# Kernel optimization log

Hardware: AMD Instinct MI355X
Metric: run time of the kernel (lower is better)

## Reference

```python
import jax, jax.numpy as jnp
import numpy as np

B, T, C, A, D, H, W = 2, 16, 64, 64, 32, 32, 32  # batch, timepoints, channels, att_features, spatial


def setup_inputs() -> dict:
    key = jax.random.key(0)
    ks = jax.random.split(key, 7)
    s = 1.0 / np.sqrt(C)
    return {
        "x": jax.random.normal(ks[0], (B, T, C, D, H, W), dtype=jnp.float32),
        "Wk": jax.random.normal(ks[1], (A, C), dtype=jnp.float32) * s,
        "bk": jax.random.normal(ks[2], (A,), dtype=jnp.float32) * s,
        "Wq": jax.random.normal(ks[3], (A, C), dtype=jnp.float32) * s,
        "bq": jax.random.normal(ks[4], (A,), dtype=jnp.float32) * s,
        "Wv": jax.random.normal(ks[5], (C, C), dtype=jnp.float32) * s,
        "bv": jax.random.normal(ks[6], (C,), dtype=jnp.float32) * s,
    }


def reference(x, Wk, bk, Wq, bq, Wv, bv):
    # kernel=1 Conv3d == pointwise channel mixing. Project and move spatial
    # dims to the front exactly like movedim((3,4,5),(1,2,3)):
    # result layout [B, D, H, W, T, out_ch].
    def proj(Wt, bt):
        return jnp.einsum('btcdhw,oc->bdhwto', x, Wt) + bt

    k = proj(Wk, bk)  # [B,D,H,W,T,A]
    q = proj(Wq, bq)  # [B,D,H,W,T,A]
    v = proj(Wv, bv)  # [B,D,H,W,T,C]

    scale = 1.0 / np.sqrt(float(Wk.shape[0]))  # sqrt(att_features)
    att = jnp.einsum('bdhwta,bdhwsa->bdhwts', k, q) * scale  # [B,D,H,W,T,T]
    # norm = partial(softmax, dim=1) on the 6-D tensor -> softmax over spatial D axis
    att_map = jax.nn.softmax(att, axis=1)

    # features = (value^T @ att_map)^T: feat[...,s,c] = sum_t v[...,t,c] * att_map[...,t,s]
    feat = jnp.einsum('bdhwtc,bdhwts->bdhwsc', v, att_map)  # [B,D,H,W,T,C]
    # movedim((1,2,3),(3,4,5)): back to [B, T, C, D, H, W]
    return jnp.transpose(feat, (0, 4, 5, 1, 2, 3))
```

## Files before the change

kernel.cpp:

```cpp
#include <hip/hip_runtime.h>
#include <hip/hip_fp16.h>

typedef short v8s __attribute__((ext_vector_type(8)));
typedef float v4f __attribute__((ext_vector_type(4)));
typedef float v2f __attribute__((ext_vector_type(2)));

#define NSP 32768
#define XSTR 2056
#define WS_ZP_B  65536ull
#define WS_ATT_B 16777216ull
#define WS_V_B   50331648ull

__device__ __forceinline__ unsigned short f2bf(float f) {
  union { float f; unsigned u; } v; v.f = f;
  unsigned r = v.u + 0x7fffu + ((v.u >> 16) & 1u);
  return (unsigned short)(r >> 16);
}
__device__ __forceinline__ unsigned pk(float a, float b) {
  return (unsigned)f2bf(a) | ((unsigned)f2bf(b) << 16);
}
__device__ __forceinline__ unsigned pkh(float a, float b) {
  union { __half2 h; unsigned u; } c; c.h = __floats2half2_rn(a, b); return c.u;
}
__device__ __forceinline__ float2 uph(unsigned u) {
  union { unsigned u; __half2 h; } c; c.u = u; return __half22float2(c.h);
}

union UF8 { v8s v; unsigned u[4]; uint4 q; };


__global__ __launch_bounds__(512) void prep_kernel(
    const float* __restrict__ Wk, const float* __restrict__ bk,
    const float* __restrict__ Wq, const float* __restrict__ bq,
    const float* __restrict__ Wv, unsigned* __restrict__ ws) {
  __shared__ float sWk[4096], sWq[4096], sWv[4096], sbk[64], sbq[64];
  for (int i = threadIdx.x; i < 4096; i += 512) { sWk[i] = Wk[i]; sWq[i] = Wq[i]; sWv[i] = Wv[i]; }
  if (threadIdx.x < 64) { sbk[threadIdx.x] = bk[threadIdx.x]; sbq[threadIdx.x] = bq[threadIdx.x]; }
  __syncthreads();
  for (int task = threadIdx.x; task < 18 * 64; task += 512) {
    int f = task >> 6, lane = task & 63;
    int i16 = lane & 15, g = lane >> 4;
    unsigned short e[8];
    #pragma unroll
    for (int j = 0; j < 8; ++j) {
      int k = (((j >> 2) << 4) + 4 * g + (j & 3));
      float acc = 0.f;
      if (f < 8) {
        int row = ((f >> 1) << 4) + i16;
        int cc  = ((f & 1) << 5) + k;
        for (int a = 0; a < 64; ++a) acc += sWk[a * 64 + row] * sWq[a * 64 + cc];
      } else if (f < 10) {
        int c = ((f - 8) << 5) + k;
        if (i16 == 0)      { for (int a = 0; a < 64; ++a) acc += sWk[a * 64 + c] * sbq[a]; }
        else if (i16 == 1) { for (int a = 0; a < 64; ++a) acc += sbk[a] * sWq[a * 64 + c]; }
      } else {
        int c  = (((f - 10) >> 1) << 4) + i16;
        int cp = (((f - 10) & 1) << 5) + k;
        acc = sWv[c * 64 + cp];
      }
      e[j] = f2bf(acc);
    }
    unsigned* dst = ws + (size_t)(f * 64 + lane) * 4;
    dst[0] = e[0] | ((unsigned)e[1] << 16);
    dst[1] = e[2] | ((unsigned)e[3] << 16);
    dst[2] = e[4] | ((unsigned)e[5] << 16);
    dst[3] = e[6] | ((unsigned)e[7] << 16);
  }
  if (threadIdx.x == 0) {
    float beta = 0.f;
    for (int a = 0; a < 64; ++a) beta += sbk[a] * sbq[a];
    ((float*)ws)[18 * 256] = beta;
  }
}

#define S2L 0.18033688011112042f

#define DECODE256() \
  int bid = (int)blockIdx.x; \
  int b = bid & 1, dc = (bid >> 1) & 3, h = bid >> 3; \
  const int d0 = dc << 3; \
  const size_t base0 = (size_t)b * 33554432 + h * 32;

#define DECODE512() \
  int bid = (int)blockIdx.x; \
  int b = bid & 1, dcc = (bid >> 1) & 7, h = bid >> 4; \
  const int d0 = dcc << 2; \
  const size_t base0 = (size_t)b * 33554432 + h * 32;

#define STAGE_DEFS() \
  const int w2 = tid & 15; \
  const int rp0 = tid >> 4; \
  v2f sA[8], sB[8]; \
  auto issueH = [&](int d, int half) { \
    const float* xp = x + base0 + (size_t)d * 1024; \
    _Pragma("unroll") \
    for (int i = 0; i < 8; ++i) { \
      int rp = half * 256 + (i << 5) + rp0; \
      const float* r0 = xp + (size_t)(2 * rp) * NSP + 2 * w2; \
      sA[i] = *(const v2f*)r0; \
      sB[i] = *(const v2f*)(r0 + NSP); \
    } \
  }; \
  auto writeH = [&](unsigned char* BUF, int half) { \
    _Pragma("unroll") \
    for (int i = 0; i < 8; ++i) { \
      int rp = half * 256 + (i << 5) + rp0; \
      int t = rp >> 5, c = (rp & 31) << 1; \
      int off = (t << 7) + (((c << 1)) ^ ((t & 7) << 4)); \
      *(unsigned*)(&BUF[(2 * w2) * XSTR + off])     = pk(sA[i].x, sB[i].x); \
      *(unsigned*)(&BUF[(2 * w2 + 1) * XSTR + off]) = pk(sA[i].y, sB[i].y); \
    } \
  };

#define LOADX_DEF() \
  auto loadX = [&](const unsigned char* BUF, int loc, v8s fX[2]) { \
    const unsigned char* bp = &BUF[loc * XSTR + (i16 << 7)]; \
    const int sw = (i16 & 7) << 4; \
    _Pragma("unroll") \
    for (int kc = 0; kc < 2; ++kc) { \
      union { v8s v; unsigned long long dd[2]; } u; \
      int o = (kc << 6) + (g << 3); \
      u.dd[0] = *(const unsigned long long*)(bp + (o ^ sw)); \
      u.dd[1] = *(const unsigned long long*)(bp + ((o + 32) ^ sw)); \
      fX[kc] = u.v; \
    } \
  };

#define LDF_DEF() \
  auto ldf = [&](int f) -> v8s { \
    union { v8s v; uint4 q; } u; \
    u.q = *(const uint4*)&Wm[(f << 8) + (lane << 2)]; \
    return u.v; \
  };

#define ATTOF_DEF() \
  auto attOf = [&](const v8s fX[2]) -> v4f { \
    v4f accW[4]; \
    _Pragma("unroll") \
    for (int tr = 0; tr < 4; ++tr) { \
      v8s m0 = ldf(2 * tr), m1 = ldf(2 * tr + 1); \
      v4f a = {0.f, 0.f, 0.f, 0.f}; \
      a = __builtin_amdgcn_mfma_f32_16x16x32_bf16(m0, fX[0], a, 0, 0, 0); \
      a = __builtin_amdgcn_mfma_f32_16x16x32_bf16(m1, fX[1], a, 0, 0, 0); \
      accW[tr] = a; \
    } \
    v8s u0 = ldf(8), u1 = ldf(9); \
    v4f au = {0.f, 0.f, 0.f, 0.f}; \
    au = __builtin_amdgcn_mfma_f32_16x16x32_bf16(u0, fX[0], au, 0, 0, 0); \
    au = __builtin_amdgcn_mfma_f32_16x16x32_bf16(u1, fX[1], au, 0, 0, 0); \
    float a1v = au[0] + beta; \
    float a2v = au[1]; \
    float a2s = __shfl(a2v, i16); \
    v4f att; \
    _Pragma("unroll") \
    for (int j = 0; j < 4; ++j) att[j] = __shfl(a1v, 4 * g + j) + a2s; \
    _Pragma("unroll") \
    for (int kc = 0; kc < 2; ++kc) { \
      UF8 w; \
      w.u[0] = pk(accW[2 * kc][0], accW[2 * kc][1]); \
      w.u[1] = pk(accW[2 * kc][2], accW[2 * kc][3]); \
      w.u[2] = pk(accW[2 * kc + 1][0], accW[2 * kc + 1][1]); \
      w.u[3] = pk(accW[2 * kc + 1][2], accW[2 * kc + 1][3]); \
      att = __builtin_amdgcn_mfma_f32_16x16x32_bf16(fX[kc], w.v, att, 0, 0, 0); \
    } \
    return att; \
  };

#define FEATQ(tn, FB) do { \
  _Pragma("unroll") \
  for (int l = 0; l < 4; ++l) { \
    int wq = 4 * wv + l; \
    UF8 fP; fP.u[0] = Pp[l][0]; fP.u[1] = Pp[l][1]; fP.u[2] = 0; fP.u[3] = 0; \
    UF8 fV; fV.u[0] = vp[l][2 * (tn)]; fV.u[1] = vp[l][2 * (tn) + 1]; fV.u[2] = 0; fV.u[3] = 0; \
    v4f ft = {0.f, 0.f, 0.f, 0.f}; \
    ft = __builtin_amdgcn_mfma_f32_16x16x32_bf16(fP.v, fV.v, ft, 0, 0, 0); \
    _Pragma("unroll") \
    for (int j = 0; j < 4; ++j) { \
      int r = (4 * g + j) * 16 + i16; \
      (FB)[r * 33 + (wq ^ g)] = ft[j]; \
    } \
  } \
} while (0)

__global__ __launch_bounds__(512) void pass1_z(
    const float* __restrict__ x, const float* __restrict__ bv,
    const unsigned* __restrict__ ws, float* __restrict__ zp,
    unsigned* __restrict__ attw, unsigned* __restrict__ vw) {
  __shared__ __align__(16) unsigned char Xd[2][65792];
  __shared__ unsigned Wm[4608];

  const int tid = (int)threadIdx.x;
  const int lane = tid & 63, wv = tid >> 6;
  const int i16 = lane & 15, g = lane >> 4;
  DECODE256();

  for (int o = tid; o < 4608; o += 512) Wm[o] = ws[o];
  const float beta = ((const float*)ws)[4608];
  float bvv[4];
  #pragma unroll
  for (int tn = 0; tn < 4; ++tn) bvv[tn] = bv[i16 + 16 * tn];

  STAGE_DEFS();
  LOADX_DEF();
  LDF_DEF();
  ATTOF_DEF();

  auto doLoc = [&](const unsigned char* cur, int d, int l, float Zl[4]) {
    v8s fX[2]; loadX(cur, 4 * wv + l, fX);
    v4f att = attOf(fX);
    float s0 = att[0] * S2L, s1 = att[1] * S2L;
    float s2 = att[2] * S2L, s3 = att[3] * S2L;
    Zl[0] += exp2f(s0); Zl[1] += exp2f(s1);
    Zl[2] += exp2f(s2); Zl[3] += exp2f(s3);
    const size_t ls = ((size_t)((b << 5) + h) * 32 + d) * 32 + (4 * wv + l);
    uint2 av; av.x = pkh(s0, s1); av.y = pkh(s2, s3);
    *(uint2*)(attw + ls * 128 + lane * 2) = av;
    uint4 o0, o1;
    {
      v4f a;
      a = (v4f){bvv[0], bvv[0], bvv[0], bvv[0]};
      a = __builtin_amdgcn_mfma_f32_16x16x32_bf16(fX[0], ldf(10), a, 0, 0, 0);
      a = __builtin_amdgcn_mfma_f32_16x16x32_bf16(fX[1], ldf(11), a, 0, 0, 0);
      o0.x = pk(a[0], a[1]); o0.y = pk(a[2], a[3]);
      a = (v4f){bvv[1], bvv[1], bvv[1], bvv[1]};
      a = __builtin_amdgcn_mfma_f32_16x16x32_bf16(fX[0], ldf(12), a, 0, 0, 0);
      a = __builtin_amdgcn_mfma_f32_16x16x32_bf16(fX[1], ldf(13), a, 0, 0, 0);
      o0.z = pk(a[0], a[1]); o0.w = pk(a[2], a[3]);
      a = (v4f){bvv[2], bvv[2], bvv[2], bvv[2]};
      a = __builtin_amdgcn_mfma_f32_16x16x32_bf16(fX[0], ldf(14), a, 0, 0, 0);
      a = __builtin_amdgcn_mfma_f32_16x16x32_bf16(fX[1], ldf(15), a, 0, 0, 0);
      o1.x = pk(a[0], a[1]); o1.y = pk(a[2], a[3]);
      a = (v4f){bvv[3], bvv[3], bvv[3], bvv[3]};
      a = __builtin_amdgcn_mfma_f32_16x16x32_bf16(fX[0], ldf(16), a, 0, 0, 0);
      a = __builtin_amdgcn_mfma_f32_16x16x32_bf16(fX[1], ldf(17), a, 0, 0, 0);
      o1.z = pk(a[0], a[1]); o1.w = pk(a[2], a[3]);
    }
    uint4* vpd = (uint4*)vw + ls * 128 + lane * 2;
    vpd[0] = o0; vpd[1] = o1;
  };

  float Z[4][4] = {};
  issueH(d0, 0); writeH(Xd[0], 0);
  issueH(d0, 1); writeH(Xd[0], 1);
  __syncthreads();
  for (int ii = 0; ii < 8; ++ii) {
    const int d = d0 + ii;
    unsigned char* cur = Xd[ii & 1];
    unsigned char* nxt = Xd[(ii & 1) ^ 1];
    if (ii < 7) issueH(d + 1, 0);
    doLoc(cur, d, 0, Z[0]);
    doLoc(cur, d, 1, Z[1]);
    if (ii < 7) { writeH(nxt, 0); issueH(d + 1, 1); }
    doLoc(cur, d, 2, Z[2]);
    doLoc(cur, d, 3, Z[3]);
    if (ii < 7) writeH(nxt, 1);
    __syncthreads();
  }
  const int locg = b * 1024 + h * 32 + 4 * wv;
  #pragma unroll
  for (int l = 0; l < 4; ++l)
    #pragma unroll
    for (int j = 0; j < 4; ++j)
      zp[(((size_t)dc * 2048 + locg + l) << 8) + (4 * g + j) * 16 + i16] = Z[l][j];
}

__global__ __launch_bounds__(512) void pass2_out(
    const float* __restrict__ zp, const unsigned* __restrict__ attw,
    const unsigned* __restrict__ vw, float* __restrict__ out) {
  __shared__ float Fb2[2][8448];

  const int tid = (int)threadIdx.x;
  const int lane = tid & 63, wv = tid >> 6;
  const int i16 = lane & 15, g = lane >> 4;
  DECODE512();

  float iZ[4][4];
  #pragma unroll
  for (int l = 0; l < 4; ++l) {
    const int locg = b * 1024 + h * 32 + 4 * wv + l;
    #pragma unroll
    for (int j = 0; j < 4; ++j) {
      float s = 0.f;
      #pragma unroll
      for (int c2 = 0; c2 < 4; ++c2)
        s += zp[(((size_t)c2 * 2048 + locg) << 8) + (4 * g + j) * 16 + i16];
      iZ[l][j] = 1.f / s;
    }
  }

  auto lsOf = [&](int d, int l) -> size_t {
    return ((size_t)((b << 5) + h) * 32 + d) * 32 + (4 * wv + l);
  };
  auto loadAtt = [&](int d, uint2* dst) {
    #pragma unroll
    for (int l = 0; l < 4; ++l)
      dst[l] = *(const uint2*)(attw + lsOf(d, l) * 128 + lane * 2);
  };
  auto loadV = [&](int d, uint4* a4, uint4* b4) {
    #pragma unroll
    for (int l = 0; l < 4; ++l) {
      const uint4* vpd = (const uint4*)vw + lsOf(d, l) * 128 + lane * 2;
      a4[l] = vpd[0]; b4[l] = vpd[1];
    }
  };

  auto storeQ = [&](int tn, int d, const float* FB) {
    float* op = out + base0 + (size_t)d * 1024 + (size_t)(16 * tn) * NSP;
    const int w4 = tid & 7, rr = tid >> 3;
    #pragma unroll
    for (int it = 0; it < 4; ++it) {
      int r = (it << 6) + rr;
      const float* fp = &FB[r * 33 + (w4 << 2)];
      float4 val;
      val.x = fp[0 ^ it]; val.y = fp[1 ^ it]; val.z = fp[2 ^ it]; val.w = fp[3 ^ it];
      *(float4*)(op + (size_t)((r >> 4) * 64 + (r & 15)) * NSP + (w4 << 2)) = val;
    }
  };

  uint2 ar[4]; uint4 vA[4], vB[4];
  loadAtt(d0, ar);
  loadV(d0, vA, vB);
  for (int ii = 0; ii < 4; ++ii) {
    const int d = d0 + ii;
    unsigned Pp[4][2], vp[4][8];
    #pragma unroll
    for (int l = 0; l < 4; ++l) {
      float2 f01 = uph(ar[l].x), f23 = uph(ar[l].y);
      float p0 = exp2f(f01.x) * iZ[l][0], p1 = exp2f(f01.y) * iZ[l][1];
      float p2 = exp2f(f23.x) * iZ[l][2], p3 = exp2f(f23.y) * iZ[l][3];
      Pp[l][0] = pk(p0, p1); Pp[l][1] = pk(p2, p3);
      vp[l][0] = vA[l].x; vp[l][1] = vA[l].y; vp[l][2] = vA[l].z; vp[l][3] = vA[l].w;
      vp[l][4] = vB[l].x; vp[l][5] = vB[l].y; vp[l][6] = vB[l].z; vp[l][7] = vB[l].w;
    }
    uint2 arN[4]; uint4 vAn[4], vBn[4];
    FEATQ(0, Fb2[0]);
    __syncthreads();
    storeQ(0, d, Fb2[0]);
    if (ii < 3) { loadAtt(d + 1, arN); loadV(d + 1, vAn, vBn); }
    FEATQ(1, Fb2[1]);
    __syncthreads();
    storeQ(1, d, Fb2[1]); FEATQ(2, Fb2[0]);
    __syncthreads();
    storeQ(2, d, Fb2[0]); FEATQ(3, Fb2[1]);
    __syncthreads();
    storeQ(3, d, Fb2[1]);
    if (ii < 3) {
      #pragma unroll
      for (int l = 0; l < 4; ++l) { ar[l] = arN[l]; vA[l] = vAn[l]; vB[l] = vBn[l]; }
    }
  }
}

extern "C" void kernel_launch(void* const* d_in, const int* in_sizes, int n_in,
                              void* d_out, int out_size, void* d_ws, size_t ws_size,
                              hipStream_t stream) {
  const float* x  = (const float*)d_in[0];
  const float* Wk = (const float*)d_in[1];
  const float* bk = (const float*)d_in[2];
  const float* Wq = (const float*)d_in[3];
  const float* bq = (const float*)d_in[4];
  const float* Wv = (const float*)d_in[5];
  const float* bv = (const float*)d_in[6];
  float* out = (float*)d_out;
  unsigned* ws = (unsigned*)d_ws;
  float*    zp   = (float*)((char*)d_ws + WS_ZP_B);
  unsigned* attw = (unsigned*)((char*)d_ws + WS_ATT_B);
  unsigned* vw   = (unsigned*)((char*)d_ws + WS_V_B);

  prep_kernel<<<1, 512, 0, stream>>>(Wk, bk, Wq, bq, Wv, ws);
  pass1_z<<<256, 512, 0, stream>>>(x, bv, ws, zp, attw, vw);
  pass2_out<<<512, 512, 0, stream>>>(zp, attw, vw, out);
}
```

Before: 273.7 us.

## Make each wave stage its own spatial columns and drop per-slice barriers

The x staging in pass1_z is remapped so each wave loads and writes exactly the four w-columns it later consumes in doLoc. That removes the inter-wave dependency on the shared buffer, so the per-iteration __syncthreads and the initial barrier after staging are removed; one barrier is added after the weight copy. Coalescing changes: each lane now reads an 8-byte pair along w with a stride across channel rows, instead of 16 lanes covering a contiguous 128-byte row. This could hurt global load efficiency, and any intra-wave ordering between LDS writes and reads now relies on wave-level execution.

```diff
diff --git a/kernel.cpp b/kernel.cpp
--- a/kernel.cpp
+++ b/kernel.cpp
@@ -87,31 +87,6 @@
   const int d0 = dcc << 2; \
   const size_t base0 = (size_t)b * 33554432 + h * 32;
 
-#define STAGE_DEFS() \
-  const int w2 = tid & 15; \
-  const int rp0 = tid >> 4; \
-  v2f sA[8], sB[8]; \
-  auto issueH = [&](int d, int half) { \
-    const float* xp = x + base0 + (size_t)d * 1024; \
-    _Pragma("unroll") \
-    for (int i = 0; i < 8; ++i) { \
-      int rp = half * 256 + (i << 5) + rp0; \
-      const float* r0 = xp + (size_t)(2 * rp) * NSP + 2 * w2; \
-      sA[i] = *(const v2f*)r0; \
-      sB[i] = *(const v2f*)(r0 + NSP); \
-    } \
-  }; \
-  auto writeH = [&](unsigned char* BUF, int half) { \
-    _Pragma("unroll") \
-    for (int i = 0; i < 8; ++i) { \
-      int rp = half * 256 + (i << 5) + rp0; \
-      int t = rp >> 5, c = (rp & 31) << 1; \
-      int off = (t << 7) + (((c << 1)) ^ ((t & 7) << 4)); \
-      *(unsigned*)(&BUF[(2 * w2) * XSTR + off])     = pk(sA[i].x, sB[i].x); \
-      *(unsigned*)(&BUF[(2 * w2 + 1) * XSTR + off]) = pk(sA[i].y, sB[i].y); \
-    } \
-  };
-
 #define LOADX_DEF() \
   auto loadX = [&](const unsigned char* BUF, int loc, v8s fX[2]) { \
     const unsigned char* bp = &BUF[loc * XSTR + (i16 << 7)]; \
@@ -199,8 +174,33 @@
   float bvv[4];
   #pragma unroll
   for (int tn = 0; tn < 4; ++tn) bvv[tn] = bv[i16 + 16 * tn];
-
-  STAGE_DEFS();
+  __syncthreads();
+
+  const int wp = lane & 1;
+  const int rq = lane >> 1;
+  const int wbase = 4 * wv + 2 * wp;
+  v2f sA[8], sB[8];
+  auto issueW = [&](int d, int half) {
+    const float* xp = x + base0 + (size_t)d * 1024 + wbase;
+    #pragma unroll
+    for (int i = 0; i < 8; ++i) {
+      int rp = ((half << 3) + i) * 32 + rq;
+      const float* r0 = xp + (size_t)(2 * rp) * NSP;
+      sA[i] = *(const v2f*)r0;
+      sB[i] = *(const v2f*)(r0 + NSP);
+    }
+  };
+  auto writeW = [&](unsigned char* BUF, int half) {
+    #pragma unroll
+    for (int i = 0; i < 8; ++i) {
+      int rp = ((half << 3) + i) * 32 + rq;
+      int t = rp >> 5, c = (rp & 31) << 1;
+      int off = (t << 7) + (((c << 1)) ^ ((t & 7) << 4));
+      *(unsigned*)(&BUF[wbase * XSTR + off])       = pk(sA[i].x, sB[i].x);
+      *(unsigned*)(&BUF[(wbase + 1) * XSTR + off]) = pk(sA[i].y, sB[i].y);
+    }
+  };
+
   LOADX_DEF();
   LDF_DEF();
   ATTOF_DEF();
@@ -240,21 +240,19 @@
   };
 
   float Z[4][4] = {};
-  issueH(d0, 0); writeH(Xd[0], 0);
-  issueH(d0, 1); writeH(Xd[0], 1);
-  __syncthreads();
+  issueW(d0, 0); writeW(Xd[0], 0);
+  issueW(d0, 1); writeW(Xd[0], 1);
   for (int ii = 0; ii < 8; ++ii) {
     const int d = d0 + ii;
     unsigned char* cur = Xd[ii & 1];
     unsigned char* nxt = Xd[(ii & 1) ^ 1];
-    if (ii < 7) issueH(d + 1, 0);
+    if (ii < 7) issueW(d + 1, 0);
     doLoc(cur, d, 0, Z[0]);
     doLoc(cur, d, 1, Z[1]);
-    if (ii < 7) { writeH(nxt, 0); issueH(d + 1, 1); }
+    if (ii < 7) { writeW(nxt, 0); issueW(d + 1, 1); }
     doLoc(cur, d, 2, Z[2]);
     doLoc(cur, d, 3, Z[3]);
-    if (ii < 7) writeH(nxt, 1);
-    __syncthreads();
+    if (ii < 7) writeW(nxt, 1);
   }
   const int locg = b * 1024 + h * 32 + 4 * wv;
   #pragma unroll
```

Result: slower. 349.6 us (+27.7%).
